# Optimization experiments

Hardware: AMD Instinct MI355X
Metric: run time of the kernel (lower is better)

Reference implementation:

```python
import jax, jax.numpy as jnp
import numpy as np

N_EMBD = 768
T_LEN = 4096
BATCH = 4
ATTN_SPAN = 256
LN_EPS = 1e-5
SCALE = float(np.sqrt(N_EMBD * ATTN_SPAN))


def _mlp(x, w1, b1, w2, b2):
    # Linear -> exact GELU -> Linear (weights stored [in, out])
    h = jax.nn.gelu(x @ w1 + b1, approximate=False)
    return h @ w2 + b2


def setup_inputs() -> dict:
    key = jax.random.key(0)
    ks = jax.random.split(key, 16)
    s = 1.0 / np.sqrt(N_EMBD)
    def lin(k):
        kw, kb = jax.random.split(k)
        w = jax.random.uniform(kw, (N_EMBD, N_EMBD), jnp.float32, -s, s)
        b = jax.random.uniform(kb, (N_EMBD,), jnp.float32, -s, s)
        return w, b
    qw1, qb1 = lin(ks[0]); qw2, qb2 = lin(ks[1])
    kw1, kb1 = lin(ks[2]); kw2, kb2 = lin(ks[3])
    vw1, vb1 = lin(ks[4]); vw2, vb2 = lin(ks[5])
    x = jax.random.normal(ks[6], (BATCH, T_LEN, N_EMBD), jnp.float32)
    return {
        'x': x,
        'qw1': qw1, 'qb1': qb1, 'qw2': qw2, 'qb2': qb2,
        'kw1': kw1, 'kb1': kb1, 'kw2': kw2, 'kb2': kb2,
        'vw1': vw1, 'vb1': vb1, 'vw2': vw2, 'vb2': vb2,
        'ln_w': jnp.ones((N_EMBD,), jnp.float32),
        'ln_b': jnp.zeros((N_EMBD,), jnp.float32),
    }


def reference(x, qw1, qb1, qw2, qb2, kw1, kb1, kw2, kb2,
              vw1, vb1, vw2, vb2, ln_w, ln_b):
    T = x.shape[1]
    q = _mlp(x, qw1, qb1, qw2, qb2)
    k = _mlp(x, kw1, kb1, kw2, kb2)
    v = _mlp(x, vw1, vb1, vw2, vb2)
    # full T x T scores then banded causal mask (no softmax), as in source
    scores = jnp.einsum('bid,bjd->bij', q, k) / SCALE
    idx = jnp.arange(T)
    diff = idx[:, None] - idx[None, :]  # i - j
    mask = ((diff >= 0) & (diff < ATTN_SPAN)).astype(scores.dtype)
    scores = scores * mask
    y = jnp.einsum('bij,bjd->bid', scores, v)
    mu = jnp.mean(y, axis=-1, keepdims=True)
    var = jnp.var(y, axis=-1, keepdims=True)
    return (y - mu) * jax.lax.rsqrt(var + LN_EPS) * ln_w + ln_b
```

## Files before the change

kernel.cpp:

```cpp
#include <hip/hip_runtime.h>

typedef _Float16 f16;
typedef _Float16 half8 __attribute__((ext_vector_type(8)));
typedef float float4v __attribute__((ext_vector_type(4)));

#define NE 768
#define N3 2304
#define TT 4096
#define NB 4
#define MM (NB*TT)
#define SPAN 256
#define JW 320

#define GLDS(g, l) __builtin_amdgcn_global_load_lds( \
    (const __attribute__((address_space(1))) void*)(g), \
    (__attribute__((address_space(3))) void*)(l), 16, 0, 0)

#define VMW(n) asm volatile("s_waitcnt vmcnt(" #n ")" ::: "memory")
#define SBAR() __builtin_amdgcn_s_barrier()
#define SCHED0() __builtin_amdgcn_sched_barrier(0)

__device__ __forceinline__ float gelu_exact(float v){
  return 0.5f * v * (1.0f + erff(v * 0.70710678118654752440f));
}

struct alignas(8) H4 { f16 a,b,c,d; };

__global__ __launch_bounds__(256) void cvt_f16_k(const float* __restrict__ in,
                                                 f16* __restrict__ out, int n){
  int i = (blockIdx.x*256 + threadIdx.x)*4;
  if (i >= n) return;
  float4 v = *(const float4*)(in + i);
  H4 o; o.a=(f16)v.x; o.b=(f16)v.y; o.c=(f16)v.z; o.d=(f16)v.w;
  *(H4*)(out + i) = o;
}

__global__ __launch_bounds__(256) void transpose_w6_k(
    const float* __restrict__ w0, const float* __restrict__ w1,
    const float* __restrict__ w2, const float* __restrict__ w3,
    const float* __restrict__ w4, const float* __restrict__ w5,
    f16* __restrict__ wt1, f16* __restrict__ wt2){
  __shared__ float tile[32][33];
  int z = blockIdx.z;
  const float* W = z==0?w0 : z==1?w1 : z==2?w2 : z==3?w3 : z==4?w4 : w5;
  f16* Wt = (z<3 ? wt1 + (size_t)z*NE*NE : wt2 + (size_t)(z-3)*NE*NE);
  int tx = threadIdx.x & 31, ty = threadIdx.x >> 5;
  int bx = blockIdx.x * 32, by = blockIdx.y * 32;
  #pragma unroll
  for (int r=0;r<32;r+=8) tile[ty+r][tx] = W[(size_t)(by+ty+r)*NE + bx + tx];
  __syncthreads();
  #pragma unroll
  for (int r=0;r<32;r+=8) Wt[(size_t)(bx+ty+r)*NE + by + tx] = (f16)tile[tx][ty+r];
}

__global__ void packb_k(const float* __restrict__ a0, const float* __restrict__ a1,
                        const float* __restrict__ a2, const float* __restrict__ c0,
                        const float* __restrict__ c1, const float* __restrict__ c2,
                        float* __restrict__ o1, float* __restrict__ o2){
  int i = blockIdx.x*256 + threadIdx.x;
  if (i < N3){
    const float* s = (i<NE) ? a0 : (i<2*NE ? a1 : a2);
    o1[i] = s[i % NE];
  } else if (i < 2*N3){
    int k = i - N3;
    const float* s = (k<NE) ? c0 : (k<2*NE ? c1 : c2);
    o2[k] = s[k % NE];
  }
}

__device__ __forceinline__ void gemm_core(
    const f16* __restrict__ A, int lda,
    const f16* __restrict__ Bt, int ldb,
    int brow, int bcol, f16* sh, float4v (&acc)[4][4])
{
  const int tid = threadIdx.x, lane = tid & 63, wave = tid >> 6;
  const int l15 = lane & 15, lk = lane >> 4;
  const int wr = (wave >> 1)*64, wc = (wave & 1)*64;

  const int srow   = wave*8 + (lane >> 3);
  const int schunk = ((lane & 7) ^ (lane >> 3))*8;
  const f16* Asrc = A  + (size_t)(brow + srow)*lda + schunk;
  const f16* Bsrc = Bt + (size_t)(bcol + srow)*ldb + schunk;
  const int wdst = wave*512;

  const int rsw0 = (lk ^ (l15 & 7))*8;
  const int rsw1 = ((4 + lk) ^ (l15 & 7))*8;

#define STAGE(buf, k0) do{ \
    f16* _a = sh + (buf)*16384 + wdst; \
    f16* _b = _a + 8192; \
    const f16* _as = Asrc + (k0); \
    const f16* _bs = Bsrc + (k0); \
    _Pragma("unroll") \
    for (int _t = 0; _t < 4; ++_t){ \
      GLDS(_as + (size_t)(_t*32)*lda, _a + _t*2048); \
      GLDS(_bs + (size_t)(_t*32)*ldb, _b + _t*2048); \
    } }while(0)

  STAGE(0, 0);
  #pragma unroll
  for (int t = 0; t < 12; ++t){
    const f16* Ac = sh + (t & 1)*16384;
    const f16* Bc = Ac + 8192;
    if (t < 11) STAGE((t+1) & 1, (t+1)*64);
    if (t < 11) { VMW(8); } else { VMW(0); }
    SBAR(); SCHED0();
    half8 af0[4], af1[4], bf0[4], bf1[4];
    #pragma unroll
    for (int i=0;i<4;++i){
      const f16* pa = Ac + (wr + i*16 + l15)*64;
      af0[i] = *(const half8*)(pa + rsw0);
      af1[i] = *(const half8*)(pa + rsw1);
      const f16* pb = Bc + (wc + i*16 + l15)*64;
      bf0[i] = *(const half8*)(pb + rsw0);
      bf1[i] = *(const half8*)(pb + rsw1);
    }
    #pragma unroll
    for (int i=0;i<4;++i)
      #pragma unroll
      for (int j=0;j<4;++j)
        acc[i][j] = __builtin_amdgcn_mfma_f32_16x16x32_f16(af0[i], bf0[j], acc[i][j], 0, 0, 0);
    #pragma unroll
    for (int i=0;i<4;++i)
      #pragma unroll
      for (int j=0;j<4;++j)
        acc[i][j] = __builtin_amdgcn_mfma_f32_16x16x32_f16(af1[i], bf1[j], acc[i][j], 0, 0, 0);
    SCHED0(); SBAR();
  }
#undef STAGE
}

__global__ __launch_bounds__(256) void gemm_l1_k(
    const f16* __restrict__ A, const f16* __restrict__ Bt,
    const float* __restrict__ bias, f16* __restrict__ Out)
{
  __shared__ f16 smem[32768];
  float4v acc[4][4]{};
  const int bid = blockIdx.x;
  const int L = (bid & 7)*288 + (bid >> 3);
  const int brow = (L/18)*128, bcol = (L%18)*128;
  gemm_core(A, NE, Bt, NE, brow, bcol, smem, acc);

  const int tid = threadIdx.x, lane = tid & 63, wave = tid >> 6;
  const int l15 = lane & 15, lk = lane >> 4;
  const int wr = (wave >> 1)*64, wc = (wave & 1)*64;
  #pragma unroll
  for (int j=0;j<4;++j){
    int col = wc + j*16 + l15;
    float bv = bias[bcol + col];
    #pragma unroll
    for (int i=0;i<4;++i){
      #pragma unroll
      for (int r=0;r<4;++r){
        int row = wr + i*16 + lk*4 + r;
        smem[row*128 + (col ^ ((row&7)<<3))] = (f16)gelu_exact(acc[i][j][r] + bv);
      }
    }
  }
  __syncthreads();
  #pragma unroll
  for (int it=0; it<8; ++it){
    int idx = tid + it*256;
    int row = idx >> 4, cc = (idx & 15)*8;
    half8 v = *(const half8*)&smem[row*128 + (cc ^ ((row&7)<<3))];
    *(half8*)(Out + (size_t)(brow + row)*N3 + bcol + cc) = v;
  }
}

__global__ __launch_bounds__(256) void gemm_l2_k(
    const f16* __restrict__ H, const f16* __restrict__ wt2_all,
    const float* __restrict__ b2_all,
    f16* __restrict__ qh, f16* __restrict__ kh, f16* __restrict__ vt)
{
  __shared__ f16 smem[32768];
  float4v acc[4][4]{};
  const int z = blockIdx.z;
  const int bid = blockIdx.x;
  const int L = (bid & 7)*96 + (bid >> 3);
  const int brow = (L/6)*128, bcol = (L%6)*128;
  gemm_core(H + z*NE, N3, wt2_all + (size_t)z*NE*NE, NE, brow, bcol, smem, acc);

  const float* bias = b2_all + z*NE;
  const int tid = threadIdx.x, lane = tid & 63, wave = tid >> 6;
  const int l15 = lane & 15, lk = lane >> 4;
  const int wr = (wave >> 1)*64, wc = (wave & 1)*64;

  if (z < 2){
    f16* Out = z ? kh : qh;
    #pragma unroll
    for (int j=0;j<4;++j){
      int col = wc + j*16 + l15;
      float bv = bias[bcol + col];
      #pragma unroll
      for (int i=0;i<4;++i){
        #pragma unroll
        for (int r=0;r<4;++r){
          int row = wr + i*16 + lk*4 + r;
          smem[row*128 + (col ^ ((row&7)<<3))] = (f16)(acc[i][j][r] + bv);
        }
      }
    }
    __syncthreads();
    #pragma unroll
    for (int it=0; it<8; ++it){
      int idx = tid + it*256;
      int row = idx >> 4, cc = (idx & 15)*8;
      half8 v = *(const half8*)&smem[row*128 + (cc ^ ((row&7)<<3))];
      *(half8*)(Out + (size_t)(brow + row)*NE + bcol + cc) = v;
    }
  } else {
    #pragma unroll
    for (int j=0;j<4;++j){
      int cl = wc + j*16 + l15;
      float bv = bias[bcol + cl];
      #pragma unroll
      for (int i=0;i<4;++i){
        int r0 = wr + i*16 + lk*4;
        H4 p; p.a = (f16)(acc[i][j][0] + bv); p.b = (f16)(acc[i][j][1] + bv);
              p.c = (f16)(acc[i][j][2] + bv); p.d = (f16)(acc[i][j][3] + bv);
        *(H4*)&smem[cl*128 + (r0 ^ ((cl&7)<<3))] = p;
      }
    }
    __syncthreads();
    int b = brow / TT, t0 = brow % TT;
    #pragma unroll
    for (int it=0; it<8; ++it){
      int idx = tid + it*256;
      int col = idx >> 4, rc = (idx & 15)*8;
      half8 v = *(const half8*)&smem[col*128 + (rc ^ ((col&7)<<3))];
      *(half8*)(vt + (size_t)b*NE*TT + (size_t)(bcol + col)*TT + t0 + rc) = v;
    }
  }
}

__global__ __launch_bounds__(256) void attn_qk_k(
    const f16* __restrict__ Q, const f16* __restrict__ K, f16* __restrict__ S)
{
  __shared__ f16 Ks[JW*40];
  const int tid = threadIdx.x, lane = tid & 63, wave = tid >> 6;
  const int l15 = lane & 15, lk = lane >> 4;
  const int qt = blockIdx.x, b = blockIdx.y;
  const int rowbase = b*TT + qt*64;
  const int jbase = qt*64 - SPAN;
  const int qrow = rowbase + wave*16;

  float4v acc[20]{};

  for (int k0 = 0; k0 < NE; k0 += 32){
    #pragma unroll
    for (int it=0; it<5; ++it){
      int idx = tid + it*256;
      int r = idx >> 2, c = (idx & 3)*8;
      int j = jbase + r;
      half8 v{};
      if (j >= 0) v = *(const half8*)(K + (size_t)(b*TT + j)*NE + k0 + c);
      *(half8*)&Ks[r*40 + c] = v;
    }
    __syncthreads();
    half8 aq = *(const half8*)(Q + (size_t)(qrow + l15)*NE + k0 + lk*8);
    #pragma unroll
    for (int f=0; f<20; ++f){
      half8 bk = *(const half8*)&Ks[(f*16 + l15)*40 + lk*8];
      acc[f] = __builtin_amdgcn_mfma_f32_16x16x32_f16(aq, bk, acc[f], 0, 0, 0);
    }
    __syncthreads();
  }
  const float inv = 1.0f / 443.40500673763256f;
  #pragma unroll
  for (int f=0; f<20; ++f){
    int c = f*16 + l15;
    int jg = jbase + c;
    #pragma unroll
    for (int r=0;r<4;++r){
      int iloc = wave*16 + lk*4 + r;
      int d = (qt*64 + iloc) - jg;
      float v = (d >= 0 && d < SPAN) ? acc[f][r]*inv : 0.0f;
      S[(size_t)(rowbase + iloc)*JW + c] = (f16)v;
    }
  }
}

__global__ __launch_bounds__(256) void attn_pv_k(
    const f16* __restrict__ S, const f16* __restrict__ Vt, float* __restrict__ Y)
{
  __shared__ f16 Vs[64*328];
  const int tid = threadIdx.x, lane = tid & 63, wave = tid >> 6;
  const int l15 = lane & 15, lk = lane >> 4;
  const int qt = blockIdx.x, dc = blockIdx.y, b = blockIdx.z;
  const int d0 = dc*64;
  const int jbase = qt*64 - SPAN;
  const int rowbase = b*TT + qt*64;

  #pragma unroll
  for (int it=0; it<10; ++it){
    int idx = tid + it*256;
    int dd = idx / 40;
    int c = (idx - dd*40)*8;
    int j = jbase + c;
    half8 v{};
    if (j >= 0) v = *(const half8*)(Vt + ((size_t)b*NE + d0 + dd)*TT + j);
    *(half8*)&Vs[dd*328 + c] = v;
  }
  __syncthreads();

  float4v acc[4]{};
  const f16* srow = S + (size_t)(rowbase + wave*16 + l15)*JW;
  #pragma unroll
  for (int kt = 0; kt < JW; kt += 32){
    half8 as = *(const half8*)(srow + kt + lk*8);
    #pragma unroll
    for (int nf=0; nf<4; ++nf){
      half8 bv = *(const half8*)&Vs[(nf*16 + l15)*328 + kt + lk*8];
      acc[nf] = __builtin_amdgcn_mfma_f32_16x16x32_f16(as, bv, acc[nf], 0, 0, 0);
    }
  }
  #pragma unroll
  for (int nf=0; nf<4; ++nf){
    #pragma unroll
    for (int r=0;r<4;++r){
      int row = rowbase + wave*16 + lk*4 + r;
      Y[(size_t)row*NE + d0 + nf*16 + l15] = acc[nf][r];
    }
  }
}

__global__ __launch_bounds__(256) void layernorm_k(
    const float* __restrict__ Y, const float* __restrict__ g,
    const float* __restrict__ be, float* __restrict__ Out)
{
  int row  = blockIdx.x*4 + (threadIdx.x >> 6);
  int lane = threadIdx.x & 63;
  const float* y = Y + (size_t)row*NE;
  float v[12], s=0.f, s2=0.f;
  #pragma unroll
  for (int i=0;i<12;++i){ v[i] = y[lane + i*64]; s += v[i]; s2 += v[i]*v[i]; }
  #pragma unroll
  for (int m=32;m>=1;m>>=1){ s += __shfl_xor(s,m,64); s2 += __shfl_xor(s2,m,64); }
  float mu  = s*(1.f/NE);
  float var = s2*(1.f/NE) - mu*mu;
  float rs  = rsqrtf(var + 1e-5f);
  float* o = Out + (size_t)row*NE;
  #pragma unroll
  for (int i=0;i<12;++i){ int c = lane + i*64; o[c] = (v[i]-mu)*rs*g[c] + be[c]; }
}

extern "C" void kernel_launch(void* const* d_in, const int* in_sizes, int n_in,
                              void* d_out, int out_size, void* d_ws, size_t ws_size,
                              hipStream_t stream)
{
  (void)in_sizes; (void)n_in; (void)out_size; (void)ws_size;
  const float* x     = (const float*)d_in[0];
  const float* w1[3] = {(const float*)d_in[1], (const float*)d_in[5], (const float*)d_in[9]};
  const float* b1[3] = {(const float*)d_in[2], (const float*)d_in[6], (const float*)d_in[10]};
  const float* w2[3] = {(const float*)d_in[3], (const float*)d_in[7], (const float*)d_in[11]};
  const float* b2[3] = {(const float*)d_in[4], (const float*)d_in[8], (const float*)d_in[12]};
  const float* lnw = (const float*)d_in[13];
  const float* lnb = (const float*)d_in[14];

  char* ws = (char*)d_ws;
  size_t off = 0;
  auto alloc = [&](size_t bytes)->void* {
    void* p = ws + off; off += (bytes + 255) & ~size_t(255); return p;
  };
  f16* xh  = (f16*)alloc((size_t)MM*NE*2);
  f16* Ha  = (f16*)alloc((size_t)MM*N3*2);
  f16* qh  = (f16*)alloc((size_t)MM*NE*2);
  f16* kh  = (f16*)alloc((size_t)MM*NE*2);
  f16* vt  = (f16*)alloc((size_t)MM*NE*2);
  f16* wt1 = (f16*)alloc((size_t)N3*NE*2);
  f16* wt2 = (f16*)alloc((size_t)N3*NE*2);
  float* b1a = (float*)alloc((size_t)N3*4);
  float* b2a = (float*)alloc((size_t)N3*4);
  f16*   sb  = xh;
  float* y   = (float*)Ha;

  cvt_f16_k<<<(MM*NE/4 + 255)/256, 256, 0, stream>>>(x, xh, MM*NE);
  transpose_w6_k<<<dim3(NE/32, NE/32, 6), 256, 0, stream>>>(
      w1[0], w1[1], w1[2], w2[0], w2[1], w2[2], wt1, wt2);
  packb_k<<<18, 256, 0, stream>>>(b1[0], b1[1], b1[2], b2[0], b2[1], b2[2], b1a, b2a);

  gemm_l1_k<<<dim3(MM/128 * N3/128), 256, 0, stream>>>(xh, wt1, b1a, Ha);
  gemm_l2_k<<<dim3(MM/128 * NE/128, 1, 3), 256, 0, stream>>>(Ha, wt2, b2a, qh, kh, vt);

  attn_qk_k<<<dim3(TT/64, NB), 256, 0, stream>>>(qh, kh, sb);
  attn_pv_k<<<dim3(TT/64, NE/64, NB), 256, 0, stream>>>(sb, vt, y);
  layernorm_k<<<MM/4, 256, 0, stream>>>(y, lnw, lnb, (float*)d_out);
}
```

Measured before the change: 408.3 us.

## Fuse QK and PV attention kernels with score tile kept in LDS

```diff
diff --git a/kernel.cpp b/kernel.cpp
--- a/kernel.cpp
+++ b/kernel.cpp
@@ -11,6 +11,7 @@
 #define MM (NB*TT)
 #define SPAN 256
 #define JW 320
+#define SLDS 328
 
 #define GLDS(g, l) __builtin_amdgcn_global_load_lds( \
     (const __attribute__((address_space(1))) void*)(g), \
@@ -233,93 +234,124 @@
   }
 }
 
-__global__ __launch_bounds__(256) void attn_qk_k(
-    const f16* __restrict__ Q, const f16* __restrict__ K, f16* __restrict__ S)
-{
-  __shared__ f16 Ks[JW*40];
+__global__ __launch_bounds__(256) void attn_fused_k(
+    const f16* __restrict__ Q, const f16* __restrict__ K,
+    const f16* __restrict__ Vt, float* __restrict__ Y)
+{
+  extern __shared__ __align__(16) f16 sh[];
+  f16* S  = sh;
+  f16* Ks = sh + 64*SLDS;
+  f16* Qs = Ks + 320*40;
+  f16* Vs = sh + 64*SLDS;
+
   const int tid = threadIdx.x, lane = tid & 63, wave = tid >> 6;
   const int l15 = lane & 15, lk = lane >> 4;
   const int qt = blockIdx.x, b = blockIdx.y;
   const int rowbase = b*TT + qt*64;
   const int jbase = qt*64 - SPAN;
-  const int qrow = rowbase + wave*16;
-
-  float4v acc[20]{};
-
-  for (int k0 = 0; k0 < NE; k0 += 32){
+  const half8 zero{};
+
+  float4v acc[4][5]{};
+  half8 kreg[5], qreg;
+  #pragma unroll
+  for (int it=0; it<5; ++it){
+    int idx = tid + it*256; int r = idx>>2, c = (idx&3)*8; int j = jbase + r;
+    kreg[it] = (j>=0) ? *(const half8*)(K + (size_t)(b*TT+j)*NE + c) : zero;
+  }
+  { int r = tid>>2, c = (tid&3)*8;
+    qreg = *(const half8*)(Q + (size_t)(rowbase + r)*NE + c); }
+
+  for (int t=0; t<24; ++t){
+    __syncthreads();
     #pragma unroll
     for (int it=0; it<5; ++it){
-      int idx = tid + it*256;
-      int r = idx >> 2, c = (idx & 3)*8;
-      int j = jbase + r;
-      half8 v{};
-      if (j >= 0) v = *(const half8*)(K + (size_t)(b*TT + j)*NE + k0 + c);
-      *(half8*)&Ks[r*40 + c] = v;
-    }
-    __syncthreads();
-    half8 aq = *(const half8*)(Q + (size_t)(qrow + l15)*NE + k0 + lk*8);
-    #pragma unroll
-    for (int f=0; f<20; ++f){
-      half8 bk = *(const half8*)&Ks[(f*16 + l15)*40 + lk*8];
-      acc[f] = __builtin_amdgcn_mfma_f32_16x16x32_f16(aq, bk, acc[f], 0, 0, 0);
-    }
-    __syncthreads();
+      int idx = tid + it*256; int r = idx>>2, c = (idx&3)*8;
+      *(half8*)&Ks[r*40 + c] = kreg[it];
+    }
+    { int r = tid>>2, c = (tid&3)*8; *(half8*)&Qs[r*40 + c] = qreg; }
+    __syncthreads();
+    if (t < 23){
+      int k0 = (t+1)*32;
+      #pragma unroll
+      for (int it=0; it<5; ++it){
+        int idx = tid + it*256; int r = idx>>2, c = (idx&3)*8; int j = jbase + r;
+        kreg[it] = (j>=0) ? *(const half8*)(K + (size_t)(b*TT+j)*NE + k0 + c) : zero;
+      }
+      { int r = tid>>2, c = (tid&3)*8;
+        qreg = *(const half8*)(Q + (size_t)(rowbase + r)*NE + k0 + c); }
+    }
+    half8 aq[4];
+    #pragma unroll
+    for (int i=0;i<4;++i) aq[i] = *(const half8*)&Qs[(i*16 + l15)*40 + lk*8];
+    #pragma unroll
+    for (int fl=0; fl<5; ++fl){
+      half8 bk = *(const half8*)&Ks[((wave*5 + fl)*16 + l15)*40 + lk*8];
+      #pragma unroll
+      for (int i=0;i<4;++i)
+        acc[i][fl] = __builtin_amdgcn_mfma_f32_16x16x32_f16(aq[i], bk, acc[i][fl], 0, 0, 0);
+    }
   }
   const float inv = 1.0f / 443.40500673763256f;
   #pragma unroll
-  for (int f=0; f<20; ++f){
-    int c = f*16 + l15;
-    int jg = jbase + c;
-    #pragma unroll
-    for (int r=0;r<4;++r){
-      int iloc = wave*16 + lk*4 + r;
-      int d = (qt*64 + iloc) - jg;
-      float v = (d >= 0 && d < SPAN) ? acc[f][r]*inv : 0.0f;
-      S[(size_t)(rowbase + iloc)*JW + c] = (f16)v;
-    }
-  }
-}
-
-__global__ __launch_bounds__(256) void attn_pv_k(
-    const f16* __restrict__ S, const f16* __restrict__ Vt, float* __restrict__ Y)
-{
-  __shared__ f16 Vs[64*328];
-  const int tid = threadIdx.x, lane = tid & 63, wave = tid >> 6;
-  const int l15 = lane & 15, lk = lane >> 4;
-  const int qt = blockIdx.x, dc = blockIdx.y, b = blockIdx.z;
-  const int d0 = dc*64;
-  const int jbase = qt*64 - SPAN;
-  const int rowbase = b*TT + qt*64;
-
+  for (int fl=0; fl<5; ++fl){
+    int jl = (wave*5 + fl)*16 + l15;
+    int jg = jbase + jl;
+    #pragma unroll
+    for (int i=0;i<4;++i){
+      #pragma unroll
+      for (int r=0;r<4;++r){
+        int iloc = i*16 + lk*4 + r;
+        int d = (qt*64 + iloc) - jg;
+        float v = (d >= 0 && d < SPAN) ? acc[i][fl][r]*inv : 0.0f;
+        S[iloc*SLDS + jl] = (f16)v;
+      }
+    }
+  }
+  __syncthreads();
+
+  half8 sreg[10];
+  #pragma unroll
+  for (int ks=0; ks<10; ++ks)
+    sreg[ks] = *(const half8*)&S[(wave*16 + l15)*SLDS + ks*32 + lk*8];
+
+  half8 vreg[10];
   #pragma unroll
   for (int it=0; it<10; ++it){
-    int idx = tid + it*256;
-    int dd = idx / 40;
-    int c = (idx - dd*40)*8;
-    int j = jbase + c;
-    half8 v{};
-    if (j >= 0) v = *(const half8*)(Vt + ((size_t)b*NE + d0 + dd)*TT + j);
-    *(half8*)&Vs[dd*328 + c] = v;
-  }
-  __syncthreads();
-
-  float4v acc[4]{};
-  const f16* srow = S + (size_t)(rowbase + wave*16 + l15)*JW;
-  #pragma unroll
-  for (int kt = 0; kt < JW; kt += 32){
-    half8 as = *(const half8*)(srow + kt + lk*8);
-    #pragma unroll
-    for (int nf=0; nf<4; ++nf){
-      half8 bv = *(const half8*)&Vs[(nf*16 + l15)*328 + kt + lk*8];
-      acc[nf] = __builtin_amdgcn_mfma_f32_16x16x32_f16(as, bv, acc[nf], 0, 0, 0);
-    }
-  }
-  #pragma unroll
-  for (int nf=0; nf<4; ++nf){
-    #pragma unroll
-    for (int r=0;r<4;++r){
-      int row = rowbase + wave*16 + lk*4 + r;
-      Y[(size_t)row*NE + d0 + nf*16 + l15] = acc[nf][r];
+    int idx = tid + it*256; int dd = idx/40, c = (idx - dd*40)*8; int j = jbase + c;
+    vreg[it] = (j>=0) ? *(const half8*)(Vt + ((size_t)b*NE + dd)*TT + j) : zero;
+  }
+  for (int cc=0; cc<12; ++cc){
+    __syncthreads();
+    #pragma unroll
+    for (int it=0; it<10; ++it){
+      int idx = tid + it*256; int dd = idx/40, c = (idx - dd*40)*8;
+      *(half8*)&Vs[dd*SLDS + c] = vreg[it];
+    }
+    __syncthreads();
+    if (cc < 11){
+      int d0n = (cc+1)*64;
+      #pragma unroll
+      for (int it=0; it<10; ++it){
+        int idx = tid + it*256; int dd = idx/40, c = (idx - dd*40)*8; int j = jbase + c;
+        vreg[it] = (j>=0) ? *(const half8*)(Vt + ((size_t)b*NE + d0n + dd)*TT + j) : zero;
+      }
+    }
+    float4v py[4]{};
+    #pragma unroll
+    for (int ks=0; ks<10; ++ks){
+      #pragma unroll
+      for (int fl=0; fl<4; ++fl){
+        half8 bv = *(const half8*)&Vs[(fl*16 + l15)*SLDS + ks*32 + lk*8];
+        py[fl] = __builtin_amdgcn_mfma_f32_16x16x32_f16(sreg[ks], bv, py[fl], 0, 0, 0);
+      }
+    }
+    int d0 = cc*64;
+    #pragma unroll
+    for (int fl=0; fl<4; ++fl){
+      #pragma unroll
+      for (int r=0;r<4;++r){
+        Y[(size_t)(rowbase + wave*16 + lk*4 + r)*NE + d0 + fl*16 + l15] = py[fl][r];
+      }
     }
   }
 }
@@ -371,8 +403,10 @@
   f16* wt2 = (f16*)alloc((size_t)N3*NE*2);
   float* b1a = (float*)alloc((size_t)N3*4);
   float* b2a = (float*)alloc((size_t)N3*4);
-  f16*   sb  = xh;
   float* y   = (float*)Ha;
+
+  hipFuncSetAttribute(reinterpret_cast<const void*>(&attn_fused_k),
+                      hipFuncAttributeMaxDynamicSharedMemorySize, 83968);
 
   cvt_f16_k<<<(MM*NE/4 + 255)/256, 256, 0, stream>>>(x, xh, MM*NE);
   transpose_w6_k<<<dim3(NE/32, NE/32, 6), 256, 0, stream>>>(
@@ -382,7 +416,6 @@
   gemm_l1_k<<<dim3(MM/128 * N3/128), 256, 0, stream>>>(xh, wt1, b1a, Ha);
   gemm_l2_k<<<dim3(MM/128 * NE/128, 1, 3), 256, 0, stream>>>(Ha, wt2, b2a, qh, kh, vt);
 
-  attn_qk_k<<<dim3(TT/64, NB), 256, 0, stream>>>(qh, kh, sb);
-  attn_pv_k<<<dim3(TT/64, NE/64, NB), 256, 0, stream>>>(sb, vt, y);
+  attn_fused_k<<<dim3(TT/64, NB), 256, 83968, stream>>>(qh, kh, vt, y);
   layernorm_k<<<MM/4, 256, 0, stream>>>(y, lnw, lnb, (float*)d_out);
 }
```

Result: faster. 371.8 us (-8.9%).
